# Optimization experiments

Measured on AMD Instinct MI355X. Metric: run time of the kernel, lower is better.

## Reference

```python
import jax, jax.numpy as jnp
import numpy as np

B, L, DMQ, DMV = 8, 1024, 512, 512
H, DK, DV, DOUT = 8, 64, 64, 512
EPS = 1e-6


def _layer_norm(x, gamma, beta):
    # LayerNorm over last dim (size H*DK or H*DV), eps=1e-6
    mu = jnp.mean(x, axis=-1, keepdims=True)
    var = jnp.mean(jnp.square(x - mu), axis=-1, keepdims=True)
    return (x - mu) * jax.lax.rsqrt(var + EPS) * gamma + beta


def setup_inputs() -> dict:
    key = jax.random.key(0)
    ks = jax.random.split(key, 20)
    s = 0.02
    return {
        "q": jax.random.normal(ks[0], (B, L, DMQ), jnp.float32),
        "k": jax.random.normal(ks[1], (B, L, DMV), jnp.float32),
        "v": jax.random.normal(ks[2], (B, L, DMV), jnp.float32),
        "Wq": jax.random.normal(ks[3], (DMQ, H * DK), jnp.float32) * s,
        "bq": jnp.zeros((H * DK,), jnp.float32),
        "Wk": jax.random.normal(ks[4], (DMV, H * DK), jnp.float32) * s,
        "bk": jnp.zeros((H * DK,), jnp.float32),
        "Wv": jax.random.normal(ks[5], (DMV, H * DV), jnp.float32) * s,
        "bv": jnp.zeros((H * DV,), jnp.float32),
        "g_q": jnp.ones((H * DK,), jnp.float32),
        "be_q": jnp.zeros((H * DK,), jnp.float32),
        "g_k": jnp.ones((H * DK,), jnp.float32),
        "be_k": jnp.zeros((H * DK,), jnp.float32),
        "g_v": jnp.ones((H * DV,), jnp.float32),
        "be_v": jnp.zeros((H * DV,), jnp.float32),
        "W1": jax.random.normal(ks[6], (H * DV, H * DV), jnp.float32) * s,
        "b1": jnp.zeros((H * DV,), jnp.float32),
        "W2": jax.random.normal(ks[7], (H * DV, DOUT), jnp.float32) * s,
        "b2": jnp.zeros((DOUT,), jnp.float32),
    }


def reference(q, k, v, Wq, bq, Wk, bk, Wv, bv, g_q, be_q, g_k, be_k, g_v, be_v, W1, b1, W2, b2):
    b, lq = q.shape[0], q.shape[1]
    qp = q @ Wq + bq                       # [B, Lq, H*DK]
    kp = k @ Wk + bk                       # [B, Lk, H*DK]
    vp = v @ Wv + bv                       # [B, Lv, H*DV]
    residual = qp.reshape(b, lq, H, DK)
    qn = _layer_norm(qp, g_q, be_q).reshape(b, lq, H, DK)
    kn = _layer_norm(kp, g_k, be_k).reshape(b, -1, H, DK)
    vn = _layer_norm(vp, g_v, be_v).reshape(b, -1, H, DV)
    # scaled dot-product attention (mask=None path)
    scores = jnp.einsum("bqhd,bkhd->bhqk", qn, kn) / jnp.sqrt(jnp.float32(DK))
    attn = jax.nn.softmax(scores, axis=-1)
    out = jnp.einsum("bhqk,bkhd->bqhd", attn, vn).reshape(b, lq, H * DV)
    # 2-layer FFN head: fc1 (ReLU) then fc2
    h = jax.nn.relu(out @ W1 + b1)
    out = h @ W2 + b2                      # [B, Lq, DOUT]
    return (out, residual)
```

## Files before the change

kernel.cpp:

```cpp
#include <hip/hip_runtime.h>
#include <hip/hip_bf16.h>
#include <stdint.h>

typedef unsigned short u16;
typedef __attribute__((ext_vector_type(8))) short bf16x8;
typedef __attribute__((ext_vector_type(4))) float f32x4;
typedef __attribute__((ext_vector_type(16))) float f32x16;

#define NR 8192
#define DM 512
#define NH 8
#define HD 64
#define LQ 1024

#define QSCALE (0.125f * 1.4426950408889634f)
#define SOFF 16.0f

__device__ __forceinline__ u16 f2b(float f) {
    union { float f; uint32_t u; } v; v.f = f;
    uint32_t r = v.u + 0x7fffu + ((v.u >> 16) & 1u);
    return (u16)(r >> 16);
}
__device__ __forceinline__ uint32_t pk2(float lo, float hi) {
    __hip_bfloat162 h = __float22bfloat162_rn(make_float2(lo, hi));
    union { __hip_bfloat162 h; uint32_t u; } c; c.h = h;
    return c.u;
}
__device__ __forceinline__ float b2f(uint32_t lo16) {
    union { uint32_t u; float f; } c; c.u = lo16 << 16; return c.f;
}

__global__ __launch_bounds__(256)
void prep_kernel(const float* __restrict__ q, const float* __restrict__ k,
                 const float* __restrict__ v, u16* __restrict__ qo,
                 u16* __restrict__ ko, u16* __restrict__ vo,
                 const float* __restrict__ W0, const float* __restrict__ W1,
                 const float* __restrict__ W2, const float* __restrict__ W3,
                 const float* __restrict__ W4,
                 u16* __restrict__ T0, u16* __restrict__ T1, u16* __restrict__ T2,
                 u16* __restrict__ T3, u16* __restrict__ T4)
{
    __shared__ float S[64][65];
    const int bid = blockIdx.x;
    if (bid < 6144) {
        const int y = bid >> 11, x = bid & 2047;
        const float* in = y == 0 ? q : y == 1 ? k : v;
        u16* out = y == 0 ? qo : y == 1 ? ko : vo;
        const int i = x * 256 + threadIdx.x;
        const float4* p = (const float4*)in + (size_t)i * 2;
        float4 a = p[0], b = p[1];
        uint4 o;
        o.x = pk2(a.x, a.y);
        o.y = pk2(a.z, a.w);
        o.z = pk2(b.x, b.y);
        o.w = pk2(b.z, b.w);
        ((uint4*)out)[i] = o;
    } else {
        const int id = bid - 6144;
        const int z = id >> 6, idx = id & 63;
        const float* W = z == 0 ? W0 : z == 1 ? W1 : z == 2 ? W2 : z == 3 ? W3 : W4;
        u16* Wt = z == 0 ? T0 : z == 1 ? T1 : z == 2 ? T2 : z == 3 ? T3 : T4;
        const int k0 = (idx >> 3) * 64, n0 = (idx & 7) * 64;
        #pragma unroll
        for (int p = 0; p < 16; ++p) {
            int i = threadIdx.x + p * 256;
            int r = i >> 6, c = i & 63;
            S[r][c] = W[(size_t)(k0 + r) * DM + n0 + c];
        }
        __syncthreads();
        #pragma unroll
        for (int p = 0; p < 16; ++p) {
            int i = threadIdx.x + p * 256;
            int r = i >> 6, c = i & 63;
            Wt[(size_t)(n0 + r) * DM + k0 + c] = f2b(S[c][r]);
        }
    }
}

__global__ __launch_bounds__(256)
void vt_kernel(const u16* __restrict__ vn, u16* __restrict__ vt)
{
    __shared__ u16 S[64][82];
    const int lt = blockIdx.x, bh = blockIdx.y;
    const int b = bh >> 3, h = bh & 7;
    const int t = threadIdx.x;
    {
        const int r = t >> 2, dc = (t & 3) * 16;
        const u16* src = vn + (size_t)(b * LQ + lt * 64 + r) * DM + h * HD + dc;
        *(uint4*)&S[r][dc]     = *(const uint4*)(src);
        *(uint4*)&S[r][dc + 8] = *(const uint4*)(src + 8);
    }
    __syncthreads();
    {
        const int d = t >> 2, lc = (t & 3) * 16;
        u16 tmp[16];
        #pragma unroll
        for (int e = 0; e < 16; ++e) tmp[e] = S[lc + e][d];
        u16* dst = vt + (((size_t)bh * HD + d) << 10) + lt * 64 + lc;
        *(uint4*)dst       = *(uint4*)&tmp[0];
        *(uint4*)(dst + 8) = *(uint4*)&tmp[8];
    }
}

__global__ __launch_bounds__(256)
void ln3_kernel(const float* __restrict__ Pq, const u16* __restrict__ Pk,
                const u16* __restrict__ Pv,
                const float* __restrict__ gq, const float* __restrict__ bq,
                const float* __restrict__ gk, const float* __restrict__ bk,
                const float* __restrict__ gv, const float* __restrict__ bv,
                u16* __restrict__ oq, u16* __restrict__ ok, u16* __restrict__ ov)
{
    const int y = blockIdx.y;
    const float* gm = y == 0 ? gq : y == 1 ? gk : gv;
    const float* be = y == 0 ? bq : y == 1 ? bk : bv;
    u16* out = y == 0 ? oq : y == 1 ? ok : ov;
    const float scale = y == 0 ? QSCALE : 1.f;

    const int row = blockIdx.x, t = threadIdx.x;
    const size_t off = (size_t)row * DM + t * 2;
    float vx, vy;
    if (y == 0) {
        float2 v = *(const float2*)(Pq + off);
        vx = v.x; vy = v.y;
    } else {
        const u16* P = y == 1 ? Pk : Pv;
        uint32_t u = *(const uint32_t*)(P + off);
        vx = b2f(u & 0xffffu); vy = b2f(u >> 16);
    }
    float s = vx + vy, s2 = vx * vx + vy * vy;
    #pragma unroll
    for (int o = 32; o; o >>= 1) { s += __shfl_down(s, o); s2 += __shfl_down(s2, o); }
    __shared__ float ss[4], ss2[4];
    if ((t & 63) == 0) { ss[t >> 6] = s; ss2[t >> 6] = s2; }
    __syncthreads();
    float S = ss[0] + ss[1] + ss[2] + ss[3];
    float S2 = ss2[0] + ss2[1] + ss2[2] + ss2[3];
    float mu = S * (1.f / DM);
    float var = S2 * (1.f / DM) - mu * mu;
    float rs = rsqrtf(var + 1e-6f);
    float g0 = gm[t * 2] * scale, g1 = gm[t * 2 + 1] * scale;
    float b0 = be[t * 2] * scale, b1 = be[t * 2 + 1] * scale;
    float o0 = (vx - mu) * rs * g0 + b0;
    float o1 = (vy - mu) * rs * g1 + b1;
    *(uint32_t*)(out + off) = pk2(o0, o1);
}

template<bool RELU, bool OUT_BF16>
__device__ __forceinline__
void gemm_body(const u16* __restrict__ A, const u16* __restrict__ Bt,
               const float* __restrict__ bias, void* __restrict__ Cout)
{
    __shared__ u16 Al[4 * 128 * 8];
    __shared__ u16 Bl[4 * 128 * 8];
    const int t = threadIdx.x;
    const int w = t >> 6, l = t & 63;
    const int m0 = blockIdx.x * 128, n0 = blockIdx.y * 128;
    const int sg = w & 3, sr = (w >> 2) * 64;
    const int wm = w >> 2, wn = w & 3;

    const u16* Ap = A  + (size_t)(m0 + sr + l) * DM + sg * 8;
    const u16* Bp = Bt + (size_t)(n0 + sr + l) * DM + sg * 8;
    const int su = (sg * 128 + sr + l) * 8;

    uint4 ga = *(const uint4*)Ap;
    uint4 gb = *(const uint4*)Bp;

    f32x4 acc[4][2];
    #pragma unroll
    for (int mi = 0; mi < 4; ++mi)
        #pragma unroll
        for (int ni = 0; ni < 2; ++ni)
            acc[mi][ni] = {0.f, 0.f, 0.f, 0.f};

    for (int kb = 0; kb < DM / 32; ++kb) {
        __syncthreads();
        *(uint4*)&Al[su] = ga;
        *(uint4*)&Bl[su] = gb;
        if (kb + 1 < DM / 32) {
            ga = *(const uint4*)(Ap + (kb + 1) * 32);
            gb = *(const uint4*)(Bp + (kb + 1) * 32);
        }
        __syncthreads();
        bf16x8 af[4], bfr[2];
        #pragma unroll
        for (int mi = 0; mi < 4; ++mi)
            af[mi] = *(const bf16x8*)&Al[((l >> 4) * 128 + wm * 64 + mi * 16 + (l & 15)) * 8];
        #pragma unroll
        for (int ni = 0; ni < 2; ++ni)
            bfr[ni] = *(const bf16x8*)&Bl[((l >> 4) * 128 + wn * 32 + ni * 16 + (l & 15)) * 8];
        #pragma unroll
        for (int mi = 0; mi < 4; ++mi)
            #pragma unroll
            for (int ni = 0; ni < 2; ++ni)
                acc[mi][ni] = __builtin_amdgcn_mfma_f32_16x16x32_bf16(af[mi], bfr[ni], acc[mi][ni], 0, 0, 0);
    }

    const int cq = l >> 4, cr = l & 15;
    #pragma unroll
    for (int mi = 0; mi < 4; ++mi) {
        const int row = m0 + wm * 64 + mi * 16 + cq * 4;
        #pragma unroll
        for (int ni = 0; ni < 2; ++ni) {
            const int col = n0 + wn * 32 + ni * 16 + cr;
            const float bb = bias[col];
            #pragma unroll
            for (int j = 0; j < 4; ++j) {
                float vv = acc[mi][ni][j] + bb;
                if (RELU) vv = fmaxf(vv, 0.f);
                if (OUT_BF16) ((u16*)Cout)[(size_t)(row + j) * DM + col] = f2b(vv);
                else          ((float*)Cout)[(size_t)(row + j) * DM + col] = vv;
            }
        }
    }
}

template<bool RELU, bool OUT_BF16>
__global__ __launch_bounds__(512)
void mfma_gemm_kernel(const u16* __restrict__ A, const u16* __restrict__ Bt,
                      const float* __restrict__ bias, void* __restrict__ Cout)
{
    gemm_body<RELU, OUT_BF16>(A, Bt, bias, Cout);
}

__global__ __launch_bounds__(512)
void gemm_qkv_kernel(const u16* __restrict__ qbf, const u16* __restrict__ kbf,
                     const u16* __restrict__ vbf,
                     const u16* __restrict__ WqT, const u16* __restrict__ WkT,
                     const u16* __restrict__ WvT,
                     const float* __restrict__ bq, const float* __restrict__ bk,
                     const float* __restrict__ bv,
                     float* __restrict__ res, u16* __restrict__ kpb,
                     u16* __restrict__ vpb)
{
    __shared__ u16 Al[4 * 128 * 8];
    __shared__ u16 Bl[4 * 128 * 8];
    const int z = blockIdx.z;
    const u16* A    = z == 0 ? qbf : z == 1 ? kbf : vbf;
    const u16* Bt   = z == 0 ? WqT : z == 1 ? WkT : WvT;
    const float* bb = z == 0 ? bq  : z == 1 ? bk  : bv;
    const bool obf  = z != 0;
    u16* ob   = z == 1 ? kpb : vpb;

    const int t = threadIdx.x;
    const int w = t >> 6, l = t & 63;
    const int m0 = blockIdx.x * 128, n0 = blockIdx.y * 128;
    const int sg = w & 3, sr = (w >> 2) * 64;
    const int wm = w >> 2, wn = w & 3;

    const u16* Ap = A  + (size_t)(m0 + sr + l) * DM + sg * 8;
    const u16* Bp = Bt + (size_t)(n0 + sr + l) * DM + sg * 8;
    const int su = (sg * 128 + sr + l) * 8;

    uint4 ga = *(const uint4*)Ap;
    uint4 gb = *(const uint4*)Bp;

    f32x4 acc[4][2];
    #pragma unroll
    for (int mi = 0; mi < 4; ++mi)
        #pragma unroll
        for (int ni = 0; ni < 2; ++ni)
            acc[mi][ni] = {0.f, 0.f, 0.f, 0.f};

    for (int kb = 0; kb < DM / 32; ++kb) {
        __syncthreads();
        *(uint4*)&Al[su] = ga;
        *(uint4*)&Bl[su] = gb;
        if (kb + 1 < DM / 32) {
            ga = *(const uint4*)(Ap + (kb + 1) * 32);
            gb = *(const uint4*)(Bp + (kb + 1) * 32);
        }
        __syncthreads();
        bf16x8 af[4], bfr[2];
        #pragma unroll
        for (int mi = 0; mi < 4; ++mi)
            af[mi] = *(const bf16x8*)&Al[((l >> 4) * 128 + wm * 64 + mi * 16 + (l & 15)) * 8];
        #pragma unroll
        for (int ni = 0; ni < 2; ++ni)
            bfr[ni] = *(const bf16x8*)&Bl[((l >> 4) * 128 + wn * 32 + ni * 16 + (l & 15)) * 8];
        #pragma unroll
        for (int mi = 0; mi < 4; ++mi)
            #pragma unroll
            for (int ni = 0; ni < 2; ++ni)
                acc[mi][ni] = __builtin_amdgcn_mfma_f32_16x16x32_bf16(af[mi], bfr[ni], acc[mi][ni], 0, 0, 0);
    }

    const int cq = l >> 4, cr = l & 15;
    #pragma unroll
    for (int mi = 0; mi < 4; ++mi) {
        const int row = m0 + wm * 64 + mi * 16 + cq * 4;
        #pragma unroll
        for (int ni = 0; ni < 2; ++ni) {
            const int col = n0 + wn * 32 + ni * 16 + cr;
            const float bbv = bb[col];
            #pragma unroll
            for (int j = 0; j < 4; ++j) {
                float vv = acc[mi][ni][j] + bbv;
                if (obf) ob[(size_t)(row + j) * DM + col] = f2b(vv);
                else     res[(size_t)(row + j) * DM + col] = vv;
            }
        }
    }
}

__global__ __launch_bounds__(256, 3)
void attn_mfma_kernel(const u16* __restrict__ qn, const u16* __restrict__ kn,
                      const u16* __restrict__ vt, u16* __restrict__ ab)
{
    __shared__ u16 Kl[2][8 * 64 * 8];
    __shared__ u16 Vl[2][8 * 64 * 8];
    __shared__ u16 Pl[4][8 * 32 * 8];

    const int t = threadIdx.x;
    const int w = t >> 6, l = t & 63;
    const int hi = l >> 5, ln = l & 31;

    const int bid = blockIdx.x;
    const int slot = bid >> 3;
    const int bh = (bid & 7) + 8 * (slot & 7);
    const int qt = slot >> 3;
    const int b = bh >> 3, h = bh & 7;

    const size_t bbase = (size_t)b * LQ * DM + h * HD;
    const int q0 = qt * 128 + w * 32;

    bf16x8 qf[4];
    {
        const u16* qp = qn + bbase + (size_t)(q0 + ln) * DM + hi * 8;
        #pragma unroll
        for (int c = 0; c < 4; ++c)
            qf[c] = *(const bf16x8*)(qp + c * 16);
    }

    const u16* Kg = kn + bbase + (size_t)(t & 63) * DM + (t >> 6) * 8;
    const u16* Vg = vt + (((size_t)bh * HD + (t >> 3)) << 10) + (t & 7) * 8;
    const int svu1 = ((t & 7) * 64 + (t >> 3)) * 8;
    const int svu2 = ((t & 7) * 64 + 32 + (t >> 3)) * 8;
    u16* Pw = &Pl[w][0];

    f32x16 oa0, oa1;
    #pragma unroll
    for (int r = 0; r < 16; ++r) { oa0[r] = 0.f; oa1[r] = 0.f; }
    float lsum = 0.f;

    *(uint4*)&Kl[0][t * 8]         = *(const uint4*)Kg;
    *(uint4*)&Kl[0][(t + 256) * 8] = *(const uint4*)(Kg + 32);
    *(uint4*)&Vl[0][svu1]          = *(const uint4*)Vg;
    *(uint4*)&Vl[0][svu2]          = *(const uint4*)(Vg + (32 << 10));
    uint4 ka1 = *(const uint4*)(Kg + (size_t)64 * DM);
    uint4 ka2 = *(const uint4*)(Kg + (size_t)64 * DM + 32);
    uint4 va1 = *(const uint4*)(Vg + 64);
    uint4 va2 = *(const uint4*)(Vg + (32 << 10) + 64);
    int cur = 0;

    for (int kt = 0; kt < 16; ++kt) {
        __syncthreads();

        f32x16 sa0, sa1;
        #pragma unroll
        for (int r = 0; r < 16; ++r) { sa0[r] = -SOFF; sa1[r] = -SOFF; }
        #pragma unroll
        for (int c = 0; c < 4; ++c) {
            bf16x8 k0 = *(const bf16x8*)&Kl[cur][((c * 2 + hi) * 64 + ln) * 8];
            bf16x8 k1 = *(const bf16x8*)&Kl[cur][((c * 2 + hi) * 64 + 32 + ln) * 8];
            sa0 = __builtin_amdgcn_mfma_f32_32x32x16_bf16(k0, qf[c], sa0, 0, 0, 0);
            sa1 = __builtin_amdgcn_mfma_f32_32x32x16_bf16(k1, qf[c], sa1, 0, 0, 0);
        }

        if (kt < 15) {
            *(uint4*)&Kl[cur ^ 1][t * 8]         = ka1;
            *(uint4*)&Kl[cur ^ 1][(t + 256) * 8] = ka2;
            *(uint4*)&Vl[cur ^ 1][svu1]          = va1;
            *(uint4*)&Vl[cur ^ 1][svu2]          = va2;
            if (kt < 14) {
                ka1 = *(const uint4*)(Kg + (size_t)(kt + 2) * 64 * DM);
                ka2 = *(const uint4*)(Kg + (size_t)(kt + 2) * 64 * DM + 32);
                va1 = *(const uint4*)(Vg + (kt + 2) * 64);
                va2 = *(const uint4*)(Vg + (32 << 10) + (kt + 2) * 64);
            }
        }

        #pragma unroll
        for (int r = 0; r < 16; ++r) {
            sa0[r] = __builtin_amdgcn_exp2f(sa0[r]);
            sa1[r] = __builtin_amdgcn_exp2f(sa1[r]);
            lsum += sa0[r] + sa1[r];
        }

        #pragma unroll
        for (int g0 = 0; g0 < 4; ++g0) {
            uint2 w0, w1;
            w0.x = pk2(sa0[4 * g0],     sa0[4 * g0 + 1]);
            w0.y = pk2(sa0[4 * g0 + 2], sa0[4 * g0 + 3]);
            w1.x = pk2(sa1[4 * g0],     sa1[4 * g0 + 1]);
            w1.y = pk2(sa1[4 * g0 + 2], sa1[4 * g0 + 3]);
            *(uint2*)&Pw[(g0 * 32 + ln) * 8 + 4 * hi]       = w0;
            *(uint2*)&Pw[((g0 + 4) * 32 + ln) * 8 + 4 * hi] = w1;
        }

        #pragma unroll
        for (int ks = 0; ks < 4; ++ks) {
            bf16x8 pa = *(const bf16x8*)&Pw[((ks * 2 + hi) * 32 + ln) * 8];
            bf16x8 v0 = *(const bf16x8*)&Vl[cur][((ks * 2 + hi) * 64 + ln) * 8];
            bf16x8 v1 = *(const bf16x8*)&Vl[cur][((ks * 2 + hi) * 64 + 32 + ln) * 8];
            oa0 = __builtin_amdgcn_mfma_f32_32x32x16_bf16(v0, pa, oa0, 0, 0, 0);
            oa1 = __builtin_amdgcn_mfma_f32_32x32x16_bf16(v1, pa, oa1, 0, 0, 0);
        }
        cur ^= 1;
    }

    lsum += __shfl_xor(lsum, 32, 64);
    const float rinv = 1.f / lsum;
    u16* op = ab + (size_t)(b * LQ + q0 + ln) * DM + h * HD;
    #pragma unroll
    for (int g = 0; g < 4; ++g) {
        uint2 s0, s1;
        s0.x = pk2(oa0[4 * g] * rinv, oa0[4 * g + 1] * rinv);
        s0.y = pk2(oa0[4 * g + 2] * rinv, oa0[4 * g + 3] * rinv);
        s1.x = pk2(oa1[4 * g] * rinv, oa1[4 * g + 1] * rinv);
        s1.y = pk2(oa1[4 * g + 2] * rinv, oa1[4 * g + 3] * rinv);
        *(uint2*)(op + 8 * g + 4 * hi)      = s0;
        *(uint2*)(op + 32 + 8 * g + 4 * hi) = s1;
    }
}

extern "C" void kernel_launch(void* const* d_in, const int* in_sizes, int n_in,
                              void* d_out, int out_size, void* d_ws, size_t ws_size,
                              hipStream_t stream)
{
    const float* q    = (const float*)d_in[0];
    const float* k    = (const float*)d_in[1];
    const float* v    = (const float*)d_in[2];
    const float* Wq   = (const float*)d_in[3];
    const float* bq   = (const float*)d_in[4];
    const float* Wk   = (const float*)d_in[5];
    const float* bk   = (const float*)d_in[6];
    const float* Wv   = (const float*)d_in[7];
    const float* bv   = (const float*)d_in[8];
    const float* g_q  = (const float*)d_in[9];
    const float* be_q = (const float*)d_in[10];
    const float* g_k  = (const float*)d_in[11];
    const float* be_k = (const float*)d_in[12];
    const float* g_v  = (const float*)d_in[13];
    const float* be_v = (const float*)d_in[14];
    const float* W1   = (const float*)d_in[15];
    const float* b1   = (const float*)d_in[16];
    const float* W2   = (const float*)d_in[17];
    const float* b2   = (const float*)d_in[18];

    float* outp = (float*)d_out;
    float* res  = outp + (size_t)NR * DM;

    char* wsb = (char*)d_ws;
    const size_t MB = 1024 * 1024;
    u16* kpb = (u16*)(wsb);
    u16* vpb = (u16*)(wsb + 8 * MB);
    u16* hbb = (u16*)(wsb + 16 * MB);
    u16* vtb = (u16*)(wsb + 24 * MB);
    u16* qbf = (u16*)(wsb + 32 * MB);
    u16* kbf = (u16*)(wsb + 40 * MB);
    u16* vbf = (u16*)(wsb + 48 * MB);
    u16* WqT = (u16*)(wsb + 56 * MB);
    u16* WkT = WqT + 512 * 512;
    u16* WvT = WkT + 512 * 512;
    u16* W1T = WvT + 512 * 512;
    u16* W2T = W1T + 512 * 512;
    u16* abb = (u16*)wsb;

    prep_kernel<<<6464, 256, 0, stream>>>(q, k, v, qbf, kbf, vbf,
                                          Wq, Wk, Wv, W1, W2,
                                          WqT, WkT, WvT, W1T, W2T);

    gemm_qkv_kernel<<<dim3(NR / 128, DM / 128, 3), 512, 0, stream>>>(
        qbf, kbf, vbf, WqT, WkT, WvT, bq, bk, bv, res, kpb, vpb);

    ln3_kernel<<<dim3(NR, 3), 256, 0, stream>>>(res, kpb, vpb,
                                                g_q, be_q, g_k, be_k, g_v, be_v,
                                                qbf, kbf, vbf);

    vt_kernel<<<dim3(16, 64), 256, 0, stream>>>(vbf, vtb);

    attn_mfma_kernel<<<512, 256, 0, stream>>>(qbf, kbf, vtb, abb);

    dim3 gg(NR / 128, DM / 128);
    mfma_gemm_kernel<true,  true ><<<gg, 512, 0, stream>>>(abb, W1T, b1, (void*)hbb);
    mfma_gemm_kernel<false, false><<<gg, 512, 0, stream>>>(hbb, W2T, b2, (void*)outp);
}
```

Before: 123.7 us.

## Fuse V layernorm with transpose into one kernel and raise MFMA wave priority

```diff
diff --git a/kernel.cpp b/kernel.cpp
--- a/kernel.cpp
+++ b/kernel.cpp
@@ -78,71 +78,118 @@
 }
 
 __global__ __launch_bounds__(256)
-void vt_kernel(const u16* __restrict__ vn, u16* __restrict__ vt)
-{
+void ln_all_kernel(const float* __restrict__ res, const u16* __restrict__ kpb,
+                   const u16* __restrict__ vpb,
+                   const float* __restrict__ gq, const float* __restrict__ bq,
+                   const float* __restrict__ gk, const float* __restrict__ bk,
+                   const float* __restrict__ gv, const float* __restrict__ bv,
+                   u16* __restrict__ oq, u16* __restrict__ ok,
+                   u16* __restrict__ vtb)
+{
+    __shared__ float ss[4], ss2[4];
     __shared__ u16 S[64][82];
-    const int lt = blockIdx.x, bh = blockIdx.y;
-    const int b = bh >> 3, h = bh & 7;
+    __shared__ float stats[64][2];
+    __shared__ float gb_[512], bb_[512];
+
+    const int bid = blockIdx.x;
     const int t = threadIdx.x;
+
+    if (bid < 16384) {
+        const int y = bid >> 13;
+        const int row = bid & 8191;
+        const float* gm = y == 0 ? gq : gk;
+        const float* be = y == 0 ? bq : bk;
+        u16* out = y == 0 ? oq : ok;
+        const float scale = y == 0 ? QSCALE : 1.f;
+
+        const size_t off = (size_t)row * DM + t * 2;
+        float vx, vy;
+        if (y == 0) {
+            float2 v = *(const float2*)(res + off);
+            vx = v.x; vy = v.y;
+        } else {
+            uint32_t u = *(const uint32_t*)(kpb + off);
+            vx = b2f(u & 0xffffu); vy = b2f(u >> 16);
+        }
+        float s = vx + vy, s2 = vx * vx + vy * vy;
+        #pragma unroll
+        for (int o = 32; o; o >>= 1) { s += __shfl_down(s, o); s2 += __shfl_down(s2, o); }
+        if ((t & 63) == 0) { ss[t >> 6] = s; ss2[t >> 6] = s2; }
+        __syncthreads();
+        float Sm = ss[0] + ss[1] + ss[2] + ss[3];
+        float S2m = ss2[0] + ss2[1] + ss2[2] + ss2[3];
+        float mu = Sm * (1.f / DM);
+        float var = S2m * (1.f / DM) - mu * mu;
+        float rs = rsqrtf(var + 1e-6f);
+        float g0 = gm[t * 2] * scale, g1 = gm[t * 2 + 1] * scale;
+        float b0 = be[t * 2] * scale, b1 = be[t * 2 + 1] * scale;
+        float o0 = (vx - mu) * rs * g0 + b0;
+        float o1 = (vy - mu) * rs * g1 + b1;
+        *(uint32_t*)(out + off) = pk2(o0, o1);
+        return;
+    }
+
+    const int id = bid - 16384;
+    const int lt = id & 15, b = id >> 4;
+
+    gb_[t]       = gv[t];
+    gb_[t + 256] = gv[t + 256];
+    bb_[t]       = bv[t];
+    bb_[t + 256] = bv[t + 256];
+
     {
-        const int r = t >> 2, dc = (t & 3) * 16;
-        const u16* src = vn + (size_t)(b * LQ + lt * 64 + r) * DM + h * HD + dc;
-        *(uint4*)&S[r][dc]     = *(const uint4*)(src);
-        *(uint4*)&S[r][dc + 8] = *(const uint4*)(src + 8);
+        const int r = t >> 2, qd = t & 3;
+        const u16* src = vpb + ((size_t)(b * LQ + lt * 64 + r)) * DM + qd * 8;
+        float s = 0.f, s2 = 0.f;
+        #pragma unroll
+        for (int p = 0; p < 16; ++p) {
+            uint4 x = *(const uint4*)(src + p * 32);
+            const uint32_t xs[4] = {x.x, x.y, x.z, x.w};
+            #pragma unroll
+            for (int e = 0; e < 4; ++e) {
+                float f0 = b2f(xs[e] & 0xffffu), f1 = b2f(xs[e] >> 16);
+                s += f0 + f1; s2 += f0 * f0 + f1 * f1;
+            }
+        }
+        s  += __shfl_xor(s, 1);  s  += __shfl_xor(s, 2);
+        s2 += __shfl_xor(s2, 1); s2 += __shfl_xor(s2, 2);
+        if (qd == 0) {
+            float mu = s * (1.f / DM);
+            float var = s2 * (1.f / DM) - mu * mu;
+            stats[r][0] = mu;
+            stats[r][1] = rsqrtf(var + 1e-6f);
+        }
     }
     __syncthreads();
-    {
-        const int d = t >> 2, lc = (t & 3) * 16;
-        u16 tmp[16];
-        #pragma unroll
-        for (int e = 0; e < 16; ++e) tmp[e] = S[lc + e][d];
-        u16* dst = vt + (((size_t)bh * HD + d) << 10) + lt * 64 + lc;
-        *(uint4*)dst       = *(uint4*)&tmp[0];
-        *(uint4*)(dst + 8) = *(uint4*)&tmp[8];
-    }
-}
-
-__global__ __launch_bounds__(256)
-void ln3_kernel(const float* __restrict__ Pq, const u16* __restrict__ Pk,
-                const u16* __restrict__ Pv,
-                const float* __restrict__ gq, const float* __restrict__ bq,
-                const float* __restrict__ gk, const float* __restrict__ bk,
-                const float* __restrict__ gv, const float* __restrict__ bv,
-                u16* __restrict__ oq, u16* __restrict__ ok, u16* __restrict__ ov)
-{
-    const int y = blockIdx.y;
-    const float* gm = y == 0 ? gq : y == 1 ? gk : gv;
-    const float* be = y == 0 ? bq : y == 1 ? bk : bv;
-    u16* out = y == 0 ? oq : y == 1 ? ok : ov;
-    const float scale = y == 0 ? QSCALE : 1.f;
-
-    const int row = blockIdx.x, t = threadIdx.x;
-    const size_t off = (size_t)row * DM + t * 2;
-    float vx, vy;
-    if (y == 0) {
-        float2 v = *(const float2*)(Pq + off);
-        vx = v.x; vy = v.y;
-    } else {
-        const u16* P = y == 1 ? Pk : Pv;
-        uint32_t u = *(const uint32_t*)(P + off);
-        vx = b2f(u & 0xffffu); vy = b2f(u >> 16);
-    }
-    float s = vx + vy, s2 = vx * vx + vy * vy;
-    #pragma unroll
-    for (int o = 32; o; o >>= 1) { s += __shfl_down(s, o); s2 += __shfl_down(s2, o); }
-    __shared__ float ss[4], ss2[4];
-    if ((t & 63) == 0) { ss[t >> 6] = s; ss2[t >> 6] = s2; }
-    __syncthreads();
-    float S = ss[0] + ss[1] + ss[2] + ss[3];
-    float S2 = ss2[0] + ss2[1] + ss2[2] + ss2[3];
-    float mu = S * (1.f / DM);
-    float var = S2 * (1.f / DM) - mu * mu;
-    float rs = rsqrtf(var + 1e-6f);
-    float g0 = gm[t * 2] * scale, g1 = gm[t * 2 + 1] * scale;
-    float b0 = be[t * 2] * scale, b1 = be[t * 2 + 1] * scale;
-    float o0 = (vx - mu) * rs * g0 + b0;
-    float o1 = (vy - mu) * rs * g1 + b1;
-    *(uint32_t*)(out + off) = pk2(o0, o1);
+
+    for (int h = 0; h < NH; ++h) {
+        {
+            const int rr = t >> 2, dc = (t & 3) * 16;
+            const u16* sp = vpb + ((size_t)(b * LQ + lt * 64 + rr)) * DM + h * 64 + dc;
+            uint4 a = *(const uint4*)sp;
+            uint4 b4 = *(const uint4*)(sp + 8);
+            const float mu = stats[rr][0], rs = stats[rr][1];
+            const uint32_t xs[8] = {a.x, a.y, a.z, a.w, b4.x, b4.y, b4.z, b4.w};
+            #pragma unroll
+            for (int e = 0; e < 8; ++e) {
+                const int c = h * 64 + dc + e * 2;
+                float f0 = (b2f(xs[e] & 0xffffu) - mu) * rs * gb_[c]     + bb_[c];
+                float f1 = (b2f(xs[e] >> 16)     - mu) * rs * gb_[c + 1] + bb_[c + 1];
+                *(uint32_t*)&S[rr][dc + e * 2] = pk2(f0, f1);
+            }
+        }
+        __syncthreads();
+        {
+            const int d = t >> 2, lc = (t & 3) * 16;
+            u16 tmp[16];
+            #pragma unroll
+            for (int e = 0; e < 16; ++e) tmp[e] = S[lc + e][d];
+            u16* dst = vtb + (((size_t)(b * NH + h) * HD + d) << 10) + lt * 64 + lc;
+            *(uint4*)dst       = *(uint4*)&tmp[0];
+            *(uint4*)(dst + 8) = *(uint4*)&tmp[8];
+        }
+        __syncthreads();
+    }
 }
 
 template<bool RELU, bool OUT_BF16>
@@ -358,6 +405,7 @@
         f32x16 sa0, sa1;
         #pragma unroll
         for (int r = 0; r < 16; ++r) { sa0[r] = -SOFF; sa1[r] = -SOFF; }
+        __builtin_amdgcn_s_setprio(1);
         #pragma unroll
         for (int c = 0; c < 4; ++c) {
             bf16x8 k0 = *(const bf16x8*)&Kl[cur][((c * 2 + hi) * 64 + ln) * 8];
@@ -365,6 +413,7 @@
             sa0 = __builtin_amdgcn_mfma_f32_32x32x16_bf16(k0, qf[c], sa0, 0, 0, 0);
             sa1 = __builtin_amdgcn_mfma_f32_32x32x16_bf16(k1, qf[c], sa1, 0, 0, 0);
         }
+        __builtin_amdgcn_s_setprio(0);
 
         if (kt < 15) {
             *(uint4*)&Kl[cur ^ 1][t * 8]         = ka1;
@@ -397,6 +446,7 @@
             *(uint2*)&Pw[((g0 + 4) * 32 + ln) * 8 + 4 * hi] = w1;
         }
 
+        __builtin_amdgcn_s_setprio(1);
         #pragma unroll
         for (int ks = 0; ks < 4; ++ks) {
             bf16x8 pa = *(const bf16x8*)&Pw[((ks * 2 + hi) * 32 + ln) * 8];
@@ -405,6 +455,7 @@
             oa0 = __builtin_amdgcn_mfma_f32_32x32x16_bf16(v0, pa, oa0, 0, 0, 0);
             oa1 = __builtin_amdgcn_mfma_f32_32x32x16_bf16(v1, pa, oa1, 0, 0, 0);
         }
+        __builtin_amdgcn_s_setprio(0);
         cur ^= 1;
     }
 
@@ -473,11 +524,9 @@
     gemm_qkv_kernel<<<dim3(NR / 128, DM / 128, 3), 512, 0, stream>>>(
         qbf, kbf, vbf, WqT, WkT, WvT, bq, bk, bv, res, kpb, vpb);
 
-    ln3_kernel<<<dim3(NR, 3), 256, 0, stream>>>(res, kpb, vpb,
-                                                g_q, be_q, g_k, be_k, g_v, be_v,
-                                                qbf, kbf, vbf);
-
-    vt_kernel<<<dim3(16, 64), 256, 0, stream>>>(vbf, vtb);
+    ln_all_kernel<<<16384 + 128, 256, 0, stream>>>(res, kpb, vpb,
+                                                   g_q, be_q, g_k, be_k, g_v, be_v,
+                                                   qbf, kbf, vtb);
 
     attn_mfma_kernel<<<512, 256, 0, stream>>>(qbf, kbf, vtb, abb);
 
```

Result: no change. 122.7 us (median of 2 runs) (-0.8%).
